# Kernel optimization log

Hardware: AMD Instinct MI355X
Metric: run time of the kernel (lower is better)

Reference implementation:

```python
import jax, jax.numpy as jnp
import numpy as np

INPUT_DIM = 512
HIDDEN_DIM = 1024
OUTPUT_DIM = 1000
BATCH = 256
SEQ_LEN = 256


def setup_inputs() -> dict:
    key = jax.random.key(0)
    ks = jax.random.split(key, 7)
    std = 1.0 / np.sqrt(HIDDEN_DIM)
    u = lambda k, shape: jax.random.uniform(k, shape, jnp.float32, -std, std)
    return {
        "x": jax.random.normal(ks[0], (BATCH, SEQ_LEN, INPUT_DIM), jnp.float32),
        "w_x2h": u(ks[1], (4 * HIDDEN_DIM, INPUT_DIM)),
        "b_x2h": u(ks[2], (4 * HIDDEN_DIM,)),
        "w_h2h": u(ks[3], (4 * HIDDEN_DIM, HIDDEN_DIM)),
        "b_h2h": u(ks[4], (4 * HIDDEN_DIM,)),
        "w_fc": u(ks[5], (OUTPUT_DIM, HIDDEN_DIM)),
        "b_fc": u(ks[6], (OUTPUT_DIM,)),
    }


def _lstm_last_hidden(x, w_x2h, b_x2h, w_h2h, b_h2h):
    B, T, D = x.shape
    H = w_h2h.shape[1]
    # Precompute input-to-hidden for all timesteps in one big GEMM: [B,T,4H]
    xg = jnp.einsum("btd,gd->btg", x, w_x2h) + b_x2h + b_h2h
    xg = jnp.swapaxes(xg, 0, 1)  # [T,B,4H] for scan

    def step(carry, xg_t):
        h, c = carry
        gates = xg_t + h @ w_h2h.T  # [B,4H]
        i, f, g, o = jnp.split(gates, 4, axis=1)
        i = jax.nn.sigmoid(i)
        f = jax.nn.sigmoid(f)
        g = jnp.tanh(g)
        o = jax.nn.sigmoid(o)
        c = c * f + i * g
        h = o * jnp.tanh(c)
        return (h, c), None

    h0 = jnp.zeros((B, H), x.dtype)
    c0 = jnp.zeros((B, H), x.dtype)
    (h_last, _), _ = jax.lax.scan(step, (h0, c0), xg)
    return h_last


def reference(x, w_x2h, b_x2h, w_h2h, b_h2h, w_fc, b_fc):
    h_last = _lstm_last_hidden(x, w_x2h, b_x2h, w_h2h, b_h2h)  # [B,H]
    return h_last @ w_fc.T + b_fc  # [B,OUTPUT_DIM]
```

## Files before the change

kernel.cpp:

```cpp
#include <hip/hip_runtime.h>

typedef __attribute__((ext_vector_type(8))) short short8;
typedef __attribute__((ext_vector_type(4))) float floatx4;

#define DIN  512
#define HSZ  1024
#define G4   4096
#define KTOT 1536
#define BQ   256
#define TT   256

#define MFMA __builtin_amdgcn_mfma_f32_16x16x32_bf16

__device__ __forceinline__ unsigned short f2bf(float f){
  unsigned int u = __float_as_uint(f);
  u += 0x7fffu + ((u >> 16) & 1u);
  return (unsigned short)(u >> 16);
}
__device__ __forceinline__ unsigned int pack2(float a, float b){
  return (unsigned int)f2bf(a) | ((unsigned int)f2bf(b) << 16);
}

__global__ void prep_wcat(const float* __restrict__ wx, const float* __restrict__ wh,
                          const float* __restrict__ bx, const float* __restrict__ bh,
                          unsigned short* __restrict__ Wcat, float* __restrict__ bias){
  int gid = blockIdx.x * blockDim.x + threadIdx.x;
  int idx = gid * 8;
  int g = idx / KTOT;
  int k = idx - g * KTOT;
  const float* src = (k < DIN) ? (wx + (size_t)g * DIN + k)
                               : (wh + (size_t)g * HSZ + (k - DIN));
  float4 f0 = *(const float4*)(src);
  float4 f1 = *(const float4*)(src + 4);
  uint4 v = make_uint4(pack2(f0.x,f0.y), pack2(f0.z,f0.w), pack2(f1.x,f1.y), pack2(f1.z,f1.w));
  *(uint4*)(Wcat + (size_t)g * KTOT + k) = v;
  if (gid < G4) bias[gid] = bx[gid] + bh[gid];
}

__global__ void prep_wfc(const float* __restrict__ wfc, unsigned short* __restrict__ Wfcb){
  int gid = blockIdx.x * blockDim.x + threadIdx.x;
  int idx = gid * 8;
  int n = idx >> 10;
  int k = idx & 1023;
  uint4 v;
  if (n < 1000){
    const float* src = wfc + (size_t)n * 1024 + k;
    float4 f0 = *(const float4*)(src);
    float4 f1 = *(const float4*)(src + 4);
    v = make_uint4(pack2(f0.x,f0.y), pack2(f0.z,f0.w), pack2(f1.x,f1.y), pack2(f1.z,f1.w));
  } else {
    v = make_uint4(0u, 0u, 0u, 0u);
  }
  *(uint4*)(Wfcb + idx) = v;
}

__global__ void prep_x(const float* __restrict__ x, unsigned short* __restrict__ xbf){
  int gid = blockIdx.x * 256 + threadIdx.x;
  int d8 = gid & 63;
  int b  = (gid >> 6) & 255;
  int t  = gid >> 14;
  const float* src = x + (((size_t)b * TT) + t) * DIN + d8 * 8;
  float4 f0 = *(const float4*)(src);
  float4 f1 = *(const float4*)(src + 4);
  uint4 v = make_uint4(pack2(f0.x,f0.y), pack2(f0.z,f0.w), pack2(f1.x,f1.y), pack2(f1.z,f1.w));
  *(uint4*)(xbf + (((size_t)t * BQ) + b) * DIN + d8 * 8) = v;
}

__global__ void init_misc(unsigned int* __restrict__ h0w, unsigned int* __restrict__ cnt, int ncnt){
  int gid = blockIdx.x * 256 + threadIdx.x;
  if (gid < 131072) h0w[gid] = 0u;
  if (gid < ncnt)   cnt[gid] = 0u;
}

__global__ __launch_bounds__(512, 2)
void lstm_persist(const unsigned short* __restrict__ xbf,
                  const unsigned short* __restrict__ Wcat,
                  const float* __restrict__ bias,
                  unsigned short* __restrict__ hseq,
                  unsigned int* __restrict__ cnt){
  extern __shared__ char smem[];
  char*  Ws  = smem;
  float* Gt2 = (float*)(smem + 98304);
  float* Bls = (float*)(smem + 98304 + 34816);

  const int tid  = threadIdx.x;
  const int bx   = blockIdx.x;
  const int bg   = bx >> 7;
  const int b0   = bg << 7;
  const int hb   = bx & 127;
  const int u0   = hb << 3;
  const int lane = tid & 63;
  const int w    = tid >> 6;
  const int rg   = w & 3;
  const int kg   = w >> 2;

  {
    int c  = tid >> 4;
    int ch = tid & 15;
    int g  = c >> 3, j = c & 7;
    const char* src = (const char*)(Wcat + (size_t)(g * HSZ + u0 + j) * KTOT);
    char* dst = Ws + c * 3072;
    int xr = j << 4;
    #pragma unroll
    for (int q = 0; q < 12; ++q){
      int k2 = ch * 192 + q * 16;
      *(uint4*)(dst + (k2 ^ xr)) = *(const uint4*)(src + k2);
    }
    if (tid < 32) Bls[tid] = bias[(size_t)(tid >> 3) * HSZ + u0 + (tid & 7)];
  }
  __syncthreads();

  const int kq8  = (lane >> 4) * 8;
  const int cA   = lane & 15;
  const int cB   = 16 + (lane & 15);
  const char* bpA = Ws + cA * 3072; const int xorA = (cA & 7) << 4;
  const char* bpB = Ws + cB * 3072; const int xorB = (cB & 7) << 4;

  const size_t rowA0 = (size_t)(b0 + rg * 32 + (lane & 15));

  const int erow = tid >> 2;
  const int eup  = (tid & 3) * 2;
  float cst0 = 0.f, cst1 = 0.f;

  for (int t = 0; t < TT; ++t){
    const unsigned short* hin  = hseq + (size_t)t * (BQ * HSZ);
    unsigned short*       hout = hseq + (size_t)(t + 1) * (BQ * HSZ);

    floatx4 acc[2][2][2];
    #pragma unroll
    for (int ab = 0; ab < 2; ++ab)
      #pragma unroll
      for (int rf = 0; rf < 2; ++rf)
        #pragma unroll
        for (int cf = 0; cf < 2; ++cf)
          acc[ab][rf][cf] = (floatx4){0.f,0.f,0.f,0.f};

    short8 X0[8], X1[8];
    {
      const unsigned short* xr0 = xbf + ((size_t)t * BQ + rowA0) * DIN + kg * 256 + kq8;
      const unsigned short* xr1 = xr0 + (size_t)16 * DIN;
      #pragma unroll
      for (int p = 0; p < 8; ++p){
        X0[p] = *(const short8*)(xr0 + p * 32);
        X1[p] = *(const short8*)(xr1 + p * 32);
      }
    }
    __builtin_amdgcn_sched_barrier(0);

    if (t > 0){
      if (tid < 64){
        const unsigned int* cp = &cnt[(((size_t)t * 2 + bg) * 8) * 16];
        const int g16 = (lane & 7) * 16;
        while (true){
          unsigned int v = __hip_atomic_load(cp + g16, __ATOMIC_RELAXED, __HIP_MEMORY_SCOPE_AGENT);
          if (__ballot(v >= 16u) == ~0ull) break;
          __builtin_amdgcn_s_sleep(1);
        }
      }
      __syncthreads();
      asm volatile("" ::: "memory");
    }

    {
      const int bbase = kg * 512 + kq8 * 2;
      short8 bA[2], bB[2];
      bA[0] = *(const short8*)(bpA + ((bbase     ) ^ xorA));
      bB[0] = *(const short8*)(bpB + ((bbase     ) ^ xorB));
      bA[1] = *(const short8*)(bpA + ((bbase + 64) ^ xorA));
      bB[1] = *(const short8*)(bpB + ((bbase + 64) ^ xorB));
      #pragma unroll
      for (int j = 0; j < 8; ++j){
        const int sl = j & 1;
        short8 b0 = bA[sl], b1 = bB[sl];
        if (j < 6){
          int bb = bbase + (j + 2) * 64;
          bA[sl] = *(const short8*)(bpA + (bb ^ xorA));
          bB[sl] = *(const short8*)(bpB + (bb ^ xorB));
        }
        acc[sl][0][0] = MFMA(X0[j], b0, acc[sl][0][0], 0, 0, 0);
        acc[sl][0][1] = MFMA(X0[j], b1, acc[sl][0][1], 0, 0, 0);
        acc[sl][1][0] = MFMA(X1[j], b0, acc[sl][1][0], 0, 0, 0);
        acc[sl][1][1] = MFMA(X1[j], b1, acc[sl][1][1], 0, 0, 0);
      }
    }

    {
      const unsigned short* hr0 = hin + rowA0 * HSZ + kg * 512 + kq8;
      const unsigned short* hr1 = hr0 + (size_t)16 * HSZ;
      short8 A0[16], A1[16];
      #pragma unroll
      for (int p = 0; p < 16; ++p){
        A0[p] = *(const short8*)(hr0 + p * 32);
        A1[p] = *(const short8*)(hr1 + p * 32);
      }
      __builtin_amdgcn_sched_barrier(0);
      const int bbase = 1024 + kg * 1024 + kq8 * 2;
      short8 bA[2], bB[2];
      bA[0] = *(const short8*)(bpA + ((bbase     ) ^ xorA));
      bB[0] = *(const short8*)(bpB + ((bbase     ) ^ xorB));
      bA[1] = *(const short8*)(bpA + ((bbase + 64) ^ xorA));
      bB[1] = *(const short8*)(bpB + ((bbase + 64) ^ xorB));
      #pragma unroll
      for (int j = 0; j < 16; ++j){
        const int sl = j & 1;
        short8 b0 = bA[sl], b1 = bB[sl];
        if (j < 14){
          int bb = bbase + (j + 2) * 64;
          bA[sl] = *(const short8*)(bpA + (bb ^ xorA));
          bB[sl] = *(const short8*)(bpB + (bb ^ xorB));
        }
        acc[sl][0][0] = MFMA(A0[j], b0, acc[sl][0][0], 0, 0, 0);
        acc[sl][0][1] = MFMA(A0[j], b1, acc[sl][0][1], 0, 0, 0);
        acc[sl][1][0] = MFMA(A1[j], b0, acc[sl][1][0], 0, 0, 0);
        acc[sl][1][1] = MFMA(A1[j], b1, acc[sl][1][1], 0, 0, 0);
      }
    }

    {
      float* gdst = Gt2 + kg * (128 * 34);
      int r0 = rg * 32 + (lane >> 4) * 4;
      #pragma unroll
      for (int rf = 0; rf < 2; ++rf){
        floatx4 g0 = acc[0][rf][0] + acc[1][rf][0];
        floatx4 g1 = acc[0][rf][1] + acc[1][rf][1];
        #pragma unroll
        for (int r = 0; r < 4; ++r){
          gdst[(r0 + rf * 16 + r) * 34 + cA] = g0[r];
          gdst[(r0 + rf * 16 + r) * 34 + cB] = g1[r];
        }
      }
    }
    __syncthreads();

    {
      const float* g0p = Gt2 + erow * 34;
      const float* g1p = g0p + 128 * 34;
      float gi0 = g0p[     eup] + g1p[     eup] + Bls[     eup];
      float gf0 = g0p[ 8 + eup] + g1p[ 8 + eup] + Bls[ 8 + eup];
      float gg0 = g0p[16 + eup] + g1p[16 + eup] + Bls[16 + eup];
      float go0 = g0p[24 + eup] + g1p[24 + eup] + Bls[24 + eup];
      float gi1 = g0p[     eup + 1] + g1p[     eup + 1] + Bls[     eup + 1];
      float gf1 = g0p[ 8 + eup + 1] + g1p[ 8 + eup + 1] + Bls[ 8 + eup + 1];
      float gg1 = g0p[16 + eup + 1] + g1p[16 + eup + 1] + Bls[16 + eup + 1];
      float go1 = g0p[24 + eup + 1] + g1p[24 + eup + 1] + Bls[24 + eup + 1];

      float iv0 = 1.f / (1.f + __expf(-gi0));
      float fv0 = 1.f / (1.f + __expf(-gf0));
      float e20 = __expf(-2.f * fmaxf(fminf(gg0, 30.f), -30.f));
      float gv0 = (1.f - e20) / (1.f + e20);
      float ov0 = 1.f / (1.f + __expf(-go0));
      float cn0 = cst0 * fv0 + iv0 * gv0;
      cst0 = cn0;
      float ec0 = __expf(-2.f * fmaxf(fminf(cn0, 30.f), -30.f));
      float hv0 = ov0 * (1.f - ec0) / (1.f + ec0);

      float iv1 = 1.f / (1.f + __expf(-gi1));
      float fv1 = 1.f / (1.f + __expf(-gf1));
      float e21 = __expf(-2.f * fmaxf(fminf(gg1, 30.f), -30.f));
      float gv1 = (1.f - e21) / (1.f + e21);
      float ov1 = 1.f / (1.f + __expf(-go1));
      float cn1 = cst1 * fv1 + iv1 * gv1;
      cst1 = cn1;
      float ec1 = __expf(-2.f * fmaxf(fminf(cn1, 30.f), -30.f));
      float hv1 = ov1 * (1.f - ec1) / (1.f + ec1);

      __hip_atomic_store((unsigned int*)(hout + (size_t)(b0 + erow) * HSZ + u0 + eup),
                         pack2(hv0, hv1), __ATOMIC_RELAXED, __HIP_MEMORY_SCOPE_AGENT);
    }
    __syncthreads();

    if (tid == 0){
      __hip_atomic_fetch_add(&cnt[(((size_t)(t + 1) * 2 + bg) * 8 + (hb >> 4)) * 16], 1u,
                             __ATOMIC_RELAXED, __HIP_MEMORY_SCOPE_AGENT);
    }
  }
}

__global__ __launch_bounds__(256, 1)
void fc_kernel(const unsigned short* __restrict__ h, const unsigned short* __restrict__ wfc,
               const float* __restrict__ bfc, float* __restrict__ out){
  int bx = blockIdx.x, tid = threadIdx.x;
  int wave = tid >> 6, lane = tid & 63;
  int row0 = (bx >> 4) * 64 + wave * 16;
  int col0 = (bx & 15) * 64;
  int lr = lane & 15, lk = (lane >> 4) * 8;
  floatx4 acc[4] = {{0.f,0.f,0.f,0.f},{0.f,0.f,0.f,0.f},{0.f,0.f,0.f,0.f},{0.f,0.f,0.f,0.f}};
  #pragma unroll 4
  for (int ks = 0; ks < 32; ++ks){
    int k = ks * 32 + lk;
    short8 a = *(const short8*)(h + (size_t)(row0 + lr) * 1024 + k);
    #pragma unroll
    for (int fj = 0; fj < 4; ++fj){
      short8 b = *(const short8*)(wfc + (size_t)(col0 + fj * 16 + lr) * 1024 + k);
      acc[fj] = MFMA(a, b, acc[fj], 0, 0, 0);
    }
  }
  #pragma unroll
  for (int fj = 0; fj < 4; ++fj){
    int col = col0 + fj * 16 + lr;
    if (col < 1000){
      #pragma unroll
      for (int r = 0; r < 4; ++r){
        int row = row0 + (lane >> 4) * 4 + r;
        out[(size_t)row * 1000 + col] = acc[fj][r] + bfc[col];
      }
    }
  }
}

extern "C" void kernel_launch(void* const* d_in, const int* in_sizes, int n_in,
                              void* d_out, int out_size, void* d_ws, size_t ws_size,
                              hipStream_t stream){
  const float* x    = (const float*)d_in[0];
  const float* wx2h = (const float*)d_in[1];
  const float* bx2h = (const float*)d_in[2];
  const float* wh2h = (const float*)d_in[3];
  const float* bh2h = (const float*)d_in[4];
  const float* wfc  = (const float*)d_in[5];
  const float* bfc  = (const float*)d_in[6];
  float* out = (float*)d_out;
  char* ws = (char*)d_ws;

  unsigned short* Wcat = (unsigned short*)(ws + 0);
  unsigned short* Wfcb = (unsigned short*)(ws + 12582912);
  float*          bias = (float*)         (ws + 14680064);
  unsigned short* xbf  = (unsigned short*)(ws + 14696448);
  unsigned short* hseq = (unsigned short*)(ws + 81805312);
  unsigned int*   cntb = (unsigned int*)  (ws + 216547328);

  (void)hipFuncSetAttribute((const void*)lstm_persist,
                            hipFuncAttributeMaxDynamicSharedMemorySize, 133376);

  hipLaunchKernelGGL(prep_wcat, dim3(3072), dim3(256), 0, stream, wx2h, wh2h, bx2h, bh2h, Wcat, bias);
  hipLaunchKernelGGL(prep_wfc,  dim3(512),  dim3(256), 0, stream, wfc, Wfcb);
  hipLaunchKernelGGL(prep_x,    dim3(16384),dim3(256), 0, stream, x, xbf);
  hipLaunchKernelGGL(init_misc, dim3(512),  dim3(256), 0, stream,
                     (unsigned int*)hseq, cntb, (int)(263168 / 4));

  hipLaunchKernelGGL(lstm_persist, dim3(256), dim3(512), 133376, stream,
                     xbf, Wcat, bias, hseq, cntb);

  hipLaunchKernelGGL(fc_kernel, dim3(64), dim3(256), 0, stream,
                     hseq + (size_t)256 * BQ * HSZ, Wfcb, bfc, out);
}
```

Baseline: 3.109 ms.

## Overlap next-step input projection with barrier wait and retile persistent LSTM

Each block now owns 64 batch rows by 16 hidden units instead of 128 rows by 8 units, and only W_h2h is kept in LDS. The input projection W_x·x for step t+1 is computed right after h_t is published, using a new k-blocked bf16 copy of W_x read from global memory, so it can overlap the wait for other blocks. Per-block atomic counters are replaced by one flag per block, and each group of 64 blocks waits on its own flags. The split-K reduction goes through LDS with an extra barrier. Costs are more global traffic for W_x every step, more LDS, and extra live registers.

```diff
diff --git a/kernel.cpp b/kernel.cpp
--- a/kernel.cpp
+++ b/kernel.cpp
@@ -37,6 +37,17 @@
   if (gid < G4) bias[gid] = bx[gid] + bh[gid];
 }
 
+__global__ void prep_wxp(const float* __restrict__ wx, unsigned short* __restrict__ WxP){
+  int gid = blockIdx.x * 256 + threadIdx.x;
+  int col = gid >> 6;
+  int kb  = gid & 63;
+  const float* src = wx + (size_t)col * DIN + kb * 8;
+  float4 f0 = *(const float4*)(src);
+  float4 f1 = *(const float4*)(src + 4);
+  uint4 v = make_uint4(pack2(f0.x,f0.y), pack2(f0.z,f0.w), pack2(f1.x,f1.y), pack2(f1.z,f1.w));
+  *(uint4*)(WxP + ((size_t)kb * G4 + col) * 8) = v;
+}
+
 __global__ void prep_wfc(const float* __restrict__ wfc, unsigned short* __restrict__ Wfcb){
   int gid = blockIdx.x * blockDim.x + threadIdx.x;
   int idx = gid * 8;
@@ -66,94 +77,106 @@
   *(uint4*)(xbf + (((size_t)t * BQ) + b) * DIN + d8 * 8) = v;
 }
 
-__global__ void init_misc(unsigned int* __restrict__ h0w, unsigned int* __restrict__ cnt, int ncnt){
+__global__ void init_misc(unsigned int* __restrict__ h0w, unsigned int* __restrict__ flags, int nflags){
   int gid = blockIdx.x * 256 + threadIdx.x;
   if (gid < 131072) h0w[gid] = 0u;
-  if (gid < ncnt)   cnt[gid] = 0u;
+  if (gid < nflags) flags[gid] = 0u;
 }
 
 __global__ __launch_bounds__(512, 2)
 void lstm_persist(const unsigned short* __restrict__ xbf,
                   const unsigned short* __restrict__ Wcat,
+                  const unsigned short* __restrict__ WxP,
                   const float* __restrict__ bias,
                   unsigned short* __restrict__ hseq,
-                  unsigned int* __restrict__ cnt){
+                  unsigned int* __restrict__ flags){
   extern __shared__ char smem[];
   char*  Ws  = smem;
-  float* Gt2 = (float*)(smem + 98304);
-  float* Bls = (float*)(smem + 98304 + 34816);
+  float* Gt  = (float*)(smem + 131072);
+  float* Bls = (float*)(smem + 148480);
 
   const int tid  = threadIdx.x;
   const int bx   = blockIdx.x;
-  const int bg   = bx >> 7;
-  const int b0   = bg << 7;
-  const int hb   = bx & 127;
-  const int u0   = hb << 3;
+  const int bg   = bx >> 6;
+  const int hb6  = bx & 63;
+  const int b0   = bg << 6;
+  const int u0   = hb6 << 4;
   const int lane = tid & 63;
   const int w    = tid >> 6;
-  const int rg   = w & 3;
-  const int kg   = w >> 2;
+  const int kg   = w & 1;
+  const int cg   = (w >> 1) & 1;
+  const int rg   = (w >> 2) & 1;
 
   {
-    int c  = tid >> 4;
-    int ch = tid & 15;
-    int g  = c >> 3, j = c & 7;
-    const char* src = (const char*)(Wcat + (size_t)(g * HSZ + u0 + j) * KTOT);
-    char* dst = Ws + c * 3072;
-    int xr = j << 4;
-    #pragma unroll
-    for (int q = 0; q < 12; ++q){
-      int k2 = ch * 192 + q * 16;
-      *(uint4*)(dst + (k2 ^ xr)) = *(const uint4*)(src + k2);
-    }
-    if (tid < 32) Bls[tid] = bias[(size_t)(tid >> 3) * HSZ + u0 + (tid & 7)];
+    int c  = tid >> 3;
+    int ch = tid & 7;
+    int g = c >> 4, uu = c & 15;
+    const char* src = (const char*)(Wcat + (size_t)(g * HSZ + u0 + uu) * KTOT + DIN);
+    char* dst = Ws + c * 2048;
+    int xr = (c & 7) << 4;
+    #pragma unroll
+    for (int q = 0; q < 16; ++q){
+      int off = ch * 256 + q * 16;
+      *(uint4*)(dst + (off ^ xr)) = *(const uint4*)(src + off);
+    }
+    if (tid < 64) Bls[tid] = bias[(size_t)(tid >> 4) * HSZ + u0 + (tid & 15)];
   }
   __syncthreads();
 
-  const int kq8  = (lane >> 4) * 8;
-  const int cA   = lane & 15;
-  const int cB   = 16 + (lane & 15);
-  const char* bpA = Ws + cA * 3072; const int xorA = (cA & 7) << 4;
-  const char* bpB = Ws + cB * 3072; const int xorB = (cB & 7) << 4;
-
-  const size_t rowA0 = (size_t)(b0 + rg * 32 + (lane & 15));
-
-  const int erow = tid >> 2;
-  const int eup  = (tid & 3) * 2;
+  const int kq8 = (lane >> 4) * 8;
+  const int c0  = cg * 32 + (lane & 15);
+  const int c1  = c0 + 16;
+  const char* bp0 = Ws + c0 * 2048; const int xr0 = (c0 & 7) << 4;
+  const char* bp1 = Ws + c1 * 2048; const int xr1 = (c1 & 7) << 4;
+  const int gcol0 = (c0 >> 4) * HSZ + u0 + (lane & 15);
+  const int gcol1 = (c1 >> 4) * HSZ + u0 + (lane & 15);
+  const int arow  = b0 + rg * 32 + (lane & 15);
+
+  const int er = tid >> 3;
+  const int up = (tid & 7) * 2;
   float cst0 = 0.f, cst1 = 0.f;
+
+  floatx4 xacc[2][2];
+
+  auto compute_x = [&](int t){
+    const unsigned short* xr0p = xbf + ((size_t)t * BQ + arow) * DIN + kg * 256 + kq8;
+    const unsigned short* xr1p = xr0p + 16 * DIN;
+    short8 XA0[8], XA1[8], XB0[8], XB1[8];
+    #pragma unroll
+    for (int j = 0; j < 8; ++j){
+      XA0[j] = *(const short8*)(xr0p + j * 32);
+      XA1[j] = *(const short8*)(xr1p + j * 32);
+      int kb = kg * 32 + j * 4 + (lane >> 4);
+      XB0[j] = *(const short8*)(WxP + ((size_t)kb * G4 + gcol0) * 8);
+      XB1[j] = *(const short8*)(WxP + ((size_t)kb * G4 + gcol1) * 8);
+    }
+    __builtin_amdgcn_sched_barrier(0);
+    #pragma unroll
+    for (int rf = 0; rf < 2; ++rf)
+      #pragma unroll
+      for (int cf = 0; cf < 2; ++cf)
+        xacc[rf][cf] = (floatx4){0.f,0.f,0.f,0.f};
+    #pragma unroll
+    for (int j = 0; j < 8; ++j){
+      xacc[0][0] = MFMA(XA0[j], XB0[j], xacc[0][0], 0, 0, 0);
+      xacc[0][1] = MFMA(XA0[j], XB1[j], xacc[0][1], 0, 0, 0);
+      xacc[1][0] = MFMA(XA1[j], XB0[j], xacc[1][0], 0, 0, 0);
+      xacc[1][1] = MFMA(XA1[j], XB1[j], xacc[1][1], 0, 0, 0);
+    }
+  };
+
+  compute_x(0);
 
   for (int t = 0; t < TT; ++t){
     const unsigned short* hin  = hseq + (size_t)t * (BQ * HSZ);
     unsigned short*       hout = hseq + (size_t)(t + 1) * (BQ * HSZ);
 
-    floatx4 acc[2][2][2];
-    #pragma unroll
-    for (int ab = 0; ab < 2; ++ab)
-      #pragma unroll
-      for (int rf = 0; rf < 2; ++rf)
-        #pragma unroll
-        for (int cf = 0; cf < 2; ++cf)
-          acc[ab][rf][cf] = (floatx4){0.f,0.f,0.f,0.f};
-
-    short8 X0[8], X1[8];
-    {
-      const unsigned short* xr0 = xbf + ((size_t)t * BQ + rowA0) * DIN + kg * 256 + kq8;
-      const unsigned short* xr1 = xr0 + (size_t)16 * DIN;
-      #pragma unroll
-      for (int p = 0; p < 8; ++p){
-        X0[p] = *(const short8*)(xr0 + p * 32);
-        X1[p] = *(const short8*)(xr1 + p * 32);
-      }
-    }
-    __builtin_amdgcn_sched_barrier(0);
-
     if (t > 0){
       if (tid < 64){
-        const unsigned int* cp = &cnt[(((size_t)t * 2 + bg) * 8) * 16];
-        const int g16 = (lane & 7) * 16;
+        const unsigned int* fp = flags + (((size_t)t * 4 + bg) << 6);
         while (true){
-          unsigned int v = __hip_atomic_load(cp + g16, __ATOMIC_RELAXED, __HIP_MEMORY_SCOPE_AGENT);
-          if (__ballot(v >= 16u) == ~0ull) break;
+          unsigned int v = __hip_atomic_load(fp + lane, __ATOMIC_RELAXED, __HIP_MEMORY_SCOPE_AGENT);
+          if (__ballot(v != 0u) == ~0ull) break;
           __builtin_amdgcn_s_sleep(1);
         }
       }
@@ -161,88 +184,83 @@
       asm volatile("" ::: "memory");
     }
 
+    floatx4 hacc[2][2];
+    #pragma unroll
+    for (int rf = 0; rf < 2; ++rf)
+      #pragma unroll
+      for (int cf = 0; cf < 2; ++cf)
+        hacc[rf][cf] = (floatx4){0.f,0.f,0.f,0.f};
     {
-      const int bbase = kg * 512 + kq8 * 2;
-      short8 bA[2], bB[2];
-      bA[0] = *(const short8*)(bpA + ((bbase     ) ^ xorA));
-      bB[0] = *(const short8*)(bpB + ((bbase     ) ^ xorB));
-      bA[1] = *(const short8*)(bpA + ((bbase + 64) ^ xorA));
-      bB[1] = *(const short8*)(bpB + ((bbase + 64) ^ xorB));
-      #pragma unroll
-      for (int j = 0; j < 8; ++j){
-        const int sl = j & 1;
-        short8 b0 = bA[sl], b1 = bB[sl];
-        if (j < 6){
-          int bb = bbase + (j + 2) * 64;
-          bA[sl] = *(const short8*)(bpA + (bb ^ xorA));
-          bB[sl] = *(const short8*)(bpB + (bb ^ xorB));
-        }
-        acc[sl][0][0] = MFMA(X0[j], b0, acc[sl][0][0], 0, 0, 0);
-        acc[sl][0][1] = MFMA(X0[j], b1, acc[sl][0][1], 0, 0, 0);
-        acc[sl][1][0] = MFMA(X1[j], b0, acc[sl][1][0], 0, 0, 0);
-        acc[sl][1][1] = MFMA(X1[j], b1, acc[sl][1][1], 0, 0, 0);
-      }
-    }
-
-    {
-      const unsigned short* hr0 = hin + rowA0 * HSZ + kg * 512 + kq8;
-      const unsigned short* hr1 = hr0 + (size_t)16 * HSZ;
-      short8 A0[16], A1[16];
+      const unsigned short* hr0 = hin + (size_t)arow * HSZ + kg * 512 + kq8;
+      const unsigned short* hr1 = hr0 + 16 * HSZ;
+      short8 HA0[16], HA1[16];
       #pragma unroll
       for (int p = 0; p < 16; ++p){
-        A0[p] = *(const short8*)(hr0 + p * 32);
-        A1[p] = *(const short8*)(hr1 + p * 32);
+        HA0[p] = *(const short8*)(hr0 + p * 32);
+        HA1[p] = *(const short8*)(hr1 + p * 32);
       }
       __builtin_amdgcn_sched_barrier(0);
-      const int bbase = 1024 + kg * 1024 + kq8 * 2;
-      short8 bA[2], bB[2];
-      bA[0] = *(const short8*)(bpA + ((bbase     ) ^ xorA));
-      bB[0] = *(const short8*)(bpB + ((bbase     ) ^ xorB));
-      bA[1] = *(const short8*)(bpA + ((bbase + 64) ^ xorA));
-      bB[1] = *(const short8*)(bpB + ((bbase + 64) ^ xorB));
+      const int kb2 = kg * 1024 + kq8 * 2;
+      short8 B0[2], B1[2];
+      B0[0] = *(const short8*)(bp0 + ((kb2     ) ^ xr0));
+      B1[0] = *(const short8*)(bp1 + ((kb2     ) ^ xr1));
+      B0[1] = *(const short8*)(bp0 + ((kb2 + 64) ^ xr0));
+      B1[1] = *(const short8*)(bp1 + ((kb2 + 64) ^ xr1));
       #pragma unroll
       for (int j = 0; j < 16; ++j){
         const int sl = j & 1;
-        short8 b0 = bA[sl], b1 = bB[sl];
+        short8 b0v = B0[sl], b1v = B1[sl];
         if (j < 14){
-          int bb = bbase + (j + 2) * 64;
-          bA[sl] = *(const short8*)(bpA + (bb ^ xorA));
-          bB[sl] = *(const short8*)(bpB + (bb ^ xorB));
+          int bb = kb2 + (j + 2) * 64;
+          B0[sl] = *(const short8*)(bp0 + (bb ^ xr0));
+          B1[sl] = *(const short8*)(bp1 + (bb ^ xr1));
         }
-        acc[sl][0][0] = MFMA(A0[j], b0, acc[sl][0][0], 0, 0, 0);
-        acc[sl][0][1] = MFMA(A0[j], b1, acc[sl][0][1], 0, 0, 0);
-        acc[sl][1][0] = MFMA(A1[j], b0, acc[sl][1][0], 0, 0, 0);
-        acc[sl][1][1] = MFMA(A1[j], b1, acc[sl][1][1], 0, 0, 0);
-      }
-    }
-
-    {
-      float* gdst = Gt2 + kg * (128 * 34);
-      int r0 = rg * 32 + (lane >> 4) * 4;
+        hacc[0][0] = MFMA(HA0[j], b0v, hacc[0][0], 0, 0, 0);
+        hacc[0][1] = MFMA(HA0[j], b1v, hacc[0][1], 0, 0, 0);
+        hacc[1][0] = MFMA(HA1[j], b0v, hacc[1][0], 0, 0, 0);
+        hacc[1][1] = MFMA(HA1[j], b1v, hacc[1][1], 0, 0, 0);
+      }
+    }
+
+    if (kg == 0){
+      int grow = rg * 32 + (lane >> 4) * 4;
       #pragma unroll
       for (int rf = 0; rf < 2; ++rf){
-        floatx4 g0 = acc[0][rf][0] + acc[1][rf][0];
-        floatx4 g1 = acc[0][rf][1] + acc[1][rf][1];
+        floatx4 gv0 = hacc[rf][0] + xacc[rf][0];
+        floatx4 gv1 = hacc[rf][1] + xacc[rf][1];
         #pragma unroll
         for (int r = 0; r < 4; ++r){
-          gdst[(r0 + rf * 16 + r) * 34 + cA] = g0[r];
-          gdst[(r0 + rf * 16 + r) * 34 + cB] = g1[r];
+          Gt[(grow + rf * 16 + r) * 68 + c0] = gv0[r];
+          Gt[(grow + rf * 16 + r) * 68 + c1] = gv1[r];
         }
       }
     }
     __syncthreads();
+    if (kg == 1){
+      int grow = rg * 32 + (lane >> 4) * 4;
+      #pragma unroll
+      for (int rf = 0; rf < 2; ++rf){
+        floatx4 gv0 = hacc[rf][0] + xacc[rf][0];
+        floatx4 gv1 = hacc[rf][1] + xacc[rf][1];
+        #pragma unroll
+        for (int r = 0; r < 4; ++r){
+          Gt[(grow + rf * 16 + r) * 68 + c0] += gv0[r];
+          Gt[(grow + rf * 16 + r) * 68 + c1] += gv1[r];
+        }
+      }
+    }
+    __syncthreads();
 
     {
-      const float* g0p = Gt2 + erow * 34;
-      const float* g1p = g0p + 128 * 34;
-      float gi0 = g0p[     eup] + g1p[     eup] + Bls[     eup];
-      float gf0 = g0p[ 8 + eup] + g1p[ 8 + eup] + Bls[ 8 + eup];
-      float gg0 = g0p[16 + eup] + g1p[16 + eup] + Bls[16 + eup];
-      float go0 = g0p[24 + eup] + g1p[24 + eup] + Bls[24 + eup];
-      float gi1 = g0p[     eup + 1] + g1p[     eup + 1] + Bls[     eup + 1];
-      float gf1 = g0p[ 8 + eup + 1] + g1p[ 8 + eup + 1] + Bls[ 8 + eup + 1];
-      float gg1 = g0p[16 + eup + 1] + g1p[16 + eup + 1] + Bls[16 + eup + 1];
-      float go1 = g0p[24 + eup + 1] + g1p[24 + eup + 1] + Bls[24 + eup + 1];
+      const float* gr = Gt + er * 68;
+      float gi0 = gr[     up] + Bls[     up];
+      float gf0 = gr[16 + up] + Bls[16 + up];
+      float gg0 = gr[32 + up] + Bls[32 + up];
+      float go0 = gr[48 + up] + Bls[48 + up];
+      float gi1 = gr[     up + 1] + Bls[     up + 1];
+      float gf1 = gr[16 + up + 1] + Bls[16 + up + 1];
+      float gg1 = gr[32 + up + 1] + Bls[32 + up + 1];
+      float go1 = gr[48 + up + 1] + Bls[48 + up + 1];
 
       float iv0 = 1.f / (1.f + __expf(-gi0));
       float fv0 = 1.f / (1.f + __expf(-gf0));
@@ -264,15 +282,16 @@
       float ec1 = __expf(-2.f * fmaxf(fminf(cn1, 30.f), -30.f));
       float hv1 = ov1 * (1.f - ec1) / (1.f + ec1);
 
-      __hip_atomic_store((unsigned int*)(hout + (size_t)(b0 + erow) * HSZ + u0 + eup),
+      __hip_atomic_store((unsigned int*)(hout + (size_t)(b0 + er) * HSZ + u0 + up),
                          pack2(hv0, hv1), __ATOMIC_RELAXED, __HIP_MEMORY_SCOPE_AGENT);
     }
     __syncthreads();
 
-    if (tid == 0){
-      __hip_atomic_fetch_add(&cnt[(((size_t)(t + 1) * 2 + bg) * 8 + (hb >> 4)) * 16], 1u,
-                             __ATOMIC_RELAXED, __HIP_MEMORY_SCOPE_AGENT);
-    }
+    if (tid == 0)
+      __hip_atomic_store(&flags[(((size_t)(t + 1) * 4 + bg) << 6) + hb6], 1u,
+                         __ATOMIC_RELAXED, __HIP_MEMORY_SCOPE_AGENT);
+
+    if (t + 1 < TT) compute_x(t + 1);
   }
 }
 
@@ -321,24 +340,26 @@
   float* out = (float*)d_out;
   char* ws = (char*)d_ws;
 
-  unsigned short* Wcat = (unsigned short*)(ws + 0);
-  unsigned short* Wfcb = (unsigned short*)(ws + 12582912);
-  float*          bias = (float*)         (ws + 14680064);
-  unsigned short* xbf  = (unsigned short*)(ws + 14696448);
-  unsigned short* hseq = (unsigned short*)(ws + 81805312);
-  unsigned int*   cntb = (unsigned int*)  (ws + 216547328);
+  unsigned short* Wcat  = (unsigned short*)(ws + 0);
+  unsigned short* Wfcb  = (unsigned short*)(ws + 12582912);
+  float*          bias  = (float*)         (ws + 14680064);
+  unsigned short* WxP   = (unsigned short*)(ws + 14696448);
+  unsigned short* xbf   = (unsigned short*)(ws + 18890752);
+  unsigned short* hseq  = (unsigned short*)(ws + 85999616);
+  unsigned int*   flags = (unsigned int*)  (ws + 220741632);
 
   (void)hipFuncSetAttribute((const void*)lstm_persist,
-                            hipFuncAttributeMaxDynamicSharedMemorySize, 133376);
+                            hipFuncAttributeMaxDynamicSharedMemorySize, 148736);
 
   hipLaunchKernelGGL(prep_wcat, dim3(3072), dim3(256), 0, stream, wx2h, wh2h, bx2h, bh2h, Wcat, bias);
+  hipLaunchKernelGGL(prep_wxp,  dim3(1024), dim3(256), 0, stream, wx2h, WxP);
   hipLaunchKernelGGL(prep_wfc,  dim3(512),  dim3(256), 0, stream, wfc, Wfcb);
   hipLaunchKernelGGL(prep_x,    dim3(16384),dim3(256), 0, stream, x, xbf);
   hipLaunchKernelGGL(init_misc, dim3(512),  dim3(256), 0, stream,
-                     (unsigned int*)hseq, cntb, (int)(263168 / 4));
-
-  hipLaunchKernelGGL(lstm_persist, dim3(256), dim3(512), 133376, stream,
-                     xbf, Wcat, bias, hseq, cntb);
+                     (unsigned int*)hseq, flags, (int)(263168 / 4));
+
+  hipLaunchKernelGGL(lstm_persist, dim3(256), dim3(512), 148736, stream,
+                     xbf, Wcat, WxP, bias, hseq, flags);
 
   hipLaunchKernelGGL(fc_kernel, dim3(64), dim3(256), 0, stream,
                      hseq + (size_t)256 * BQ * HSZ, Wfcb, bfc, out);
```

Result: slower. 3.437 ms (+10.5%).

## Precompute next step's input projection off the critical path; use per-block step flags

Applied to the files above, without the earlier changes.

The x-projection MFMAs for step t+1 now run right after a block publishes its h for step t, so they overlap with waiting on other blocks instead of sitting inside the dependent chain. The grid barrier changes from per-step atomic counters to per-block monotonic step flags written with plain stores. One wave polls all 128 flags and releases the other waves through a shared-memory mailbox rather than __syncthreads. The wave-to-row/k mapping also changes (kg/rg swapped). The risk is extra live accumulator registers, and spinning waves that contend for issue slots.

```diff
diff --git a/kernel.cpp b/kernel.cpp
--- a/kernel.cpp
+++ b/kernel.cpp
@@ -66,10 +66,10 @@
   *(uint4*)(xbf + (((size_t)t * BQ) + b) * DIN + d8 * 8) = v;
 }
 
-__global__ void init_misc(unsigned int* __restrict__ h0w, unsigned int* __restrict__ cnt, int ncnt){
+__global__ void init_misc(unsigned int* __restrict__ h0w, unsigned int* __restrict__ flags, int nflags){
   int gid = blockIdx.x * 256 + threadIdx.x;
   if (gid < 131072) h0w[gid] = 0u;
-  if (gid < ncnt)   cnt[gid] = 0u;
+  if (gid < nflags) flags[gid] = 0u;
 }
 
 __global__ __launch_bounds__(512, 2)
@@ -77,11 +77,12 @@
                   const unsigned short* __restrict__ Wcat,
                   const float* __restrict__ bias,
                   unsigned short* __restrict__ hseq,
-                  unsigned int* __restrict__ cnt){
+                  unsigned int* __restrict__ flags){
   extern __shared__ char smem[];
   char*  Ws  = smem;
   float* Gt2 = (float*)(smem + 98304);
   float* Bls = (float*)(smem + 98304 + 34816);
+  __shared__ int mbx;
 
   const int tid  = threadIdx.x;
   const int bx   = blockIdx.x;
@@ -91,128 +92,137 @@
   const int u0   = hb << 3;
   const int lane = tid & 63;
   const int w    = tid >> 6;
-  const int rg   = w & 3;
-  const int kg   = w >> 2;
+  const int kg   = w & 1;
+  const int rg   = w >> 1;
 
   {
     int c  = tid >> 4;
     int ch = tid & 15;
-    int g  = c >> 3, j = c & 7;
-    const char* src = (const char*)(Wcat + (size_t)(g * HSZ + u0 + j) * KTOT);
+    int grow = (c >> 3) * HSZ + u0 + (c & 7);
+    const char* src = (const char*)(Wcat + (size_t)grow * KTOT);
     char* dst = Ws + c * 3072;
-    int xr = j << 4;
+    int xr = (c & 7) << 4;
     #pragma unroll
     for (int q = 0; q < 12; ++q){
       int k2 = ch * 192 + q * 16;
       *(uint4*)(dst + (k2 ^ xr)) = *(const uint4*)(src + k2);
     }
     if (tid < 32) Bls[tid] = bias[(size_t)(tid >> 3) * HSZ + u0 + (tid & 7)];
+    if (tid == 0) mbx = 0;
   }
   __syncthreads();
 
-  const int kq8  = (lane >> 4) * 8;
-  const int cA   = lane & 15;
-  const int cB   = 16 + (lane & 15);
+  const int kq8 = (lane >> 4) * 8;
+  const int cA  = lane & 15;
+  const int cB  = 16 + (lane & 15);
   const char* bpA = Ws + cA * 3072; const int xorA = (cA & 7) << 4;
   const char* bpB = Ws + cB * 3072; const int xorB = (cB & 7) << 4;
 
   const size_t rowA0 = (size_t)(b0 + rg * 32 + (lane & 15));
 
-  const int erow = tid >> 2;
-  const int eup  = (tid & 3) * 2;
+  const int er = tid >> 2;
+  const int up = (tid & 3) * 2;
   float cst0 = 0.f, cst1 = 0.f;
+
+  floatx4 xacc[2][2];
+
+  auto compute_x = [&](int t){
+    const unsigned short* xr0p = xbf + ((size_t)t * BQ + rowA0) * DIN + kg * 256 + kq8;
+    const unsigned short* xr1p = xr0p + 16 * DIN;
+    short8 X0[8], X1[8];
+    #pragma unroll
+    for (int p = 0; p < 8; ++p){
+      X0[p] = *(const short8*)(xr0p + p * 32);
+      X1[p] = *(const short8*)(xr1p + p * 32);
+    }
+    __builtin_amdgcn_sched_barrier(0);
+    #pragma unroll
+    for (int rf = 0; rf < 2; ++rf)
+      #pragma unroll
+      for (int cf = 0; cf < 2; ++cf)
+        xacc[rf][cf] = (floatx4){0.f,0.f,0.f,0.f};
+    const int bbase = kg * 512 + kq8 * 2;
+    short8 bA[2], bB[2];
+    bA[0] = *(const short8*)(bpA + ((bbase     ) ^ xorA));
+    bB[0] = *(const short8*)(bpB + ((bbase     ) ^ xorB));
+    bA[1] = *(const short8*)(bpA + ((bbase + 64) ^ xorA));
+    bB[1] = *(const short8*)(bpB + ((bbase + 64) ^ xorB));
+    #pragma unroll
+    for (int j = 0; j < 8; ++j){
+      const int sl = j & 1;
+      short8 b0v = bA[sl], b1v = bB[sl];
+      if (j < 6){
+        int bb = bbase + (j + 2) * 64;
+        bA[sl] = *(const short8*)(bpA + (bb ^ xorA));
+        bB[sl] = *(const short8*)(bpB + (bb ^ xorB));
+      }
+      xacc[0][0] = MFMA(X0[j], b0v, xacc[0][0], 0, 0, 0);
+      xacc[0][1] = MFMA(X0[j], b1v, xacc[0][1], 0, 0, 0);
+      xacc[1][0] = MFMA(X1[j], b0v, xacc[1][0], 0, 0, 0);
+      xacc[1][1] = MFMA(X1[j], b1v, xacc[1][1], 0, 0, 0);
+    }
+  };
+
+  compute_x(0);
+
+  const unsigned int* fz = flags + (bg << 7);
 
   for (int t = 0; t < TT; ++t){
     const unsigned short* hin  = hseq + (size_t)t * (BQ * HSZ);
     unsigned short*       hout = hseq + (size_t)(t + 1) * (BQ * HSZ);
 
-    floatx4 acc[2][2][2];
-    #pragma unroll
-    for (int ab = 0; ab < 2; ++ab)
-      #pragma unroll
-      for (int rf = 0; rf < 2; ++rf)
-        #pragma unroll
-        for (int cf = 0; cf < 2; ++cf)
-          acc[ab][rf][cf] = (floatx4){0.f,0.f,0.f,0.f};
-
-    short8 X0[8], X1[8];
-    {
-      const unsigned short* xr0 = xbf + ((size_t)t * BQ + rowA0) * DIN + kg * 256 + kq8;
-      const unsigned short* xr1 = xr0 + (size_t)16 * DIN;
-      #pragma unroll
-      for (int p = 0; p < 8; ++p){
-        X0[p] = *(const short8*)(xr0 + p * 32);
-        X1[p] = *(const short8*)(xr1 + p * 32);
-      }
-    }
-    __builtin_amdgcn_sched_barrier(0);
-
     if (t > 0){
-      if (tid < 64){
-        const unsigned int* cp = &cnt[(((size_t)t * 2 + bg) * 8) * 16];
-        const int g16 = (lane & 7) * 16;
+      if (w == 0){
         while (true){
-          unsigned int v = __hip_atomic_load(cp + g16, __ATOMIC_RELAXED, __HIP_MEMORY_SCOPE_AGENT);
-          if (__ballot(v >= 16u) == ~0ull) break;
+          unsigned int va = __hip_atomic_load(fz + lane,      __ATOMIC_RELAXED, __HIP_MEMORY_SCOPE_AGENT);
+          unsigned int vb = __hip_atomic_load(fz + 64 + lane, __ATOMIC_RELAXED, __HIP_MEMORY_SCOPE_AGENT);
+          if (__ballot(va >= (unsigned)t && vb >= (unsigned)t) == ~0ull) break;
           __builtin_amdgcn_s_sleep(1);
         }
-      }
-      __syncthreads();
+        if (lane == 0)
+          __hip_atomic_store(&mbx, t, __ATOMIC_RELAXED, __HIP_MEMORY_SCOPE_WORKGROUP);
+      } else {
+        while (__hip_atomic_load(&mbx, __ATOMIC_RELAXED, __HIP_MEMORY_SCOPE_WORKGROUP) < t)
+          __builtin_amdgcn_s_sleep(1);
+      }
       asm volatile("" ::: "memory");
     }
 
+    floatx4 hacc[2][2];
+    #pragma unroll
+    for (int rf = 0; rf < 2; ++rf)
+      #pragma unroll
+      for (int cf = 0; cf < 2; ++cf)
+        hacc[rf][cf] = (floatx4){0.f,0.f,0.f,0.f};
     {
-      const int bbase = kg * 512 + kq8 * 2;
+      const unsigned short* hr0 = hin + rowA0 * HSZ + kg * 512 + kq8;
+      const unsigned short* hr1 = hr0 + 16 * HSZ;
+      short8 HA0[16], HA1[16];
+      #pragma unroll
+      for (int p = 0; p < 16; ++p){
+        HA0[p] = *(const short8*)(hr0 + p * 32);
+        HA1[p] = *(const short8*)(hr1 + p * 32);
+      }
+      __builtin_amdgcn_sched_barrier(0);
+      const int kb2 = 1024 + kg * 1024 + kq8 * 2;
       short8 bA[2], bB[2];
-      bA[0] = *(const short8*)(bpA + ((bbase     ) ^ xorA));
-      bB[0] = *(const short8*)(bpB + ((bbase     ) ^ xorB));
-      bA[1] = *(const short8*)(bpA + ((bbase + 64) ^ xorA));
-      bB[1] = *(const short8*)(bpB + ((bbase + 64) ^ xorB));
-      #pragma unroll
-      for (int j = 0; j < 8; ++j){
+      bA[0] = *(const short8*)(bpA + ((kb2     ) ^ xorA));
+      bB[0] = *(const short8*)(bpB + ((kb2     ) ^ xorB));
+      bA[1] = *(const short8*)(bpA + ((kb2 + 64) ^ xorA));
+      bB[1] = *(const short8*)(bpB + ((kb2 + 64) ^ xorB));
+      #pragma unroll
+      for (int j = 0; j < 16; ++j){
         const int sl = j & 1;
-        short8 b0 = bA[sl], b1 = bB[sl];
-        if (j < 6){
-          int bb = bbase + (j + 2) * 64;
+        short8 b0v = bA[sl], b1v = bB[sl];
+        if (j < 14){
+          int bb = kb2 + (j + 2) * 64;
           bA[sl] = *(const short8*)(bpA + (bb ^ xorA));
           bB[sl] = *(const short8*)(bpB + (bb ^ xorB));
         }
-        acc[sl][0][0] = MFMA(X0[j], b0, acc[sl][0][0], 0, 0, 0);
-        acc[sl][0][1] = MFMA(X0[j], b1, acc[sl][0][1], 0, 0, 0);
-        acc[sl][1][0] = MFMA(X1[j], b0, acc[sl][1][0], 0, 0, 0);
-        acc[sl][1][1] = MFMA(X1[j], b1, acc[sl][1][1], 0, 0, 0);
-      }
-    }
-
-    {
-      const unsigned short* hr0 = hin + rowA0 * HSZ + kg * 512 + kq8;
-      const unsigned short* hr1 = hr0 + (size_t)16 * HSZ;
-      short8 A0[16], A1[16];
-      #pragma unroll
-      for (int p = 0; p < 16; ++p){
-        A0[p] = *(const short8*)(hr0 + p * 32);
-        A1[p] = *(const short8*)(hr1 + p * 32);
-      }
-      __builtin_amdgcn_sched_barrier(0);
-      const int bbase = 1024 + kg * 1024 + kq8 * 2;
-      short8 bA[2], bB[2];
-      bA[0] = *(const short8*)(bpA + ((bbase     ) ^ xorA));
-      bB[0] = *(const short8*)(bpB + ((bbase     ) ^ xorB));
-      bA[1] = *(const short8*)(bpA + ((bbase + 64) ^ xorA));
-      bB[1] = *(const short8*)(bpB + ((bbase + 64) ^ xorB));
-      #pragma unroll
-      for (int j = 0; j < 16; ++j){
-        const int sl = j & 1;
-        short8 b0 = bA[sl], b1 = bB[sl];
-        if (j < 14){
-          int bb = bbase + (j + 2) * 64;
-          bA[sl] = *(const short8*)(bpA + (bb ^ xorA));
-          bB[sl] = *(const short8*)(bpB + (bb ^ xorB));
-        }
-        acc[sl][0][0] = MFMA(A0[j], b0, acc[sl][0][0], 0, 0, 0);
-        acc[sl][0][1] = MFMA(A0[j], b1, acc[sl][0][1], 0, 0, 0);
-        acc[sl][1][0] = MFMA(A1[j], b0, acc[sl][1][0], 0, 0, 0);
-        acc[sl][1][1] = MFMA(A1[j], b1, acc[sl][1][1], 0, 0, 0);
+        hacc[0][0] = MFMA(HA0[j], b0v, hacc[0][0], 0, 0, 0);
+        hacc[0][1] = MFMA(HA0[j], b1v, hacc[0][1], 0, 0, 0);
+        hacc[1][0] = MFMA(HA1[j], b0v, hacc[1][0], 0, 0, 0);
+        hacc[1][1] = MFMA(HA1[j], b1v, hacc[1][1], 0, 0, 0);
       }
     }
 
@@ -221,8 +231,8 @@
       int r0 = rg * 32 + (lane >> 4) * 4;
       #pragma unroll
       for (int rf = 0; rf < 2; ++rf){
-        floatx4 g0 = acc[0][rf][0] + acc[1][rf][0];
-        floatx4 g1 = acc[0][rf][1] + acc[1][rf][1];
+        floatx4 g0 = hacc[rf][0] + xacc[rf][0];
+        floatx4 g1 = hacc[rf][1] + xacc[rf][1];
         #pragma unroll
         for (int r = 0; r < 4; ++r){
           gdst[(r0 + rf * 16 + r) * 34 + cA] = g0[r];
@@ -233,16 +243,16 @@
     __syncthreads();
 
     {
-      const float* g0p = Gt2 + erow * 34;
+      const float* g0p = Gt2 + er * 34;
       const float* g1p = g0p + 128 * 34;
-      float gi0 = g0p[     eup] + g1p[     eup] + Bls[     eup];
-      float gf0 = g0p[ 8 + eup] + g1p[ 8 + eup] + Bls[ 8 + eup];
-      float gg0 = g0p[16 + eup] + g1p[16 + eup] + Bls[16 + eup];
-      float go0 = g0p[24 + eup] + g1p[24 + eup] + Bls[24 + eup];
-      float gi1 = g0p[     eup + 1] + g1p[     eup + 1] + Bls[     eup + 1];
-      float gf1 = g0p[ 8 + eup + 1] + g1p[ 8 + eup + 1] + Bls[ 8 + eup + 1];
-      float gg1 = g0p[16 + eup + 1] + g1p[16 + eup + 1] + Bls[16 + eup + 1];
-      float go1 = g0p[24 + eup + 1] + g1p[24 + eup + 1] + Bls[24 + eup + 1];
+      float gi0 = g0p[     up] + g1p[     up] + Bls[     up];
+      float gf0 = g0p[ 8 + up] + g1p[ 8 + up] + Bls[ 8 + up];
+      float gg0 = g0p[16 + up] + g1p[16 + up] + Bls[16 + up];
+      float go0 = g0p[24 + up] + g1p[24 + up] + Bls[24 + up];
+      float gi1 = g0p[     up + 1] + g1p[     up + 1] + Bls[     up + 1];
+      float gf1 = g0p[ 8 + up + 1] + g1p[ 8 + up + 1] + Bls[ 8 + up + 1];
+      float gg1 = g0p[16 + up + 1] + g1p[16 + up + 1] + Bls[16 + up + 1];
+      float go1 = g0p[24 + up + 1] + g1p[24 + up + 1] + Bls[24 + up + 1];
 
       float iv0 = 1.f / (1.f + __expf(-gi0));
       float fv0 = 1.f / (1.f + __expf(-gf0));
@@ -264,15 +274,16 @@
       float ec1 = __expf(-2.f * fmaxf(fminf(cn1, 30.f), -30.f));
       float hv1 = ov1 * (1.f - ec1) / (1.f + ec1);
 
-      __hip_atomic_store((unsigned int*)(hout + (size_t)(b0 + erow) * HSZ + u0 + eup),
+      __hip_atomic_store((unsigned int*)(hout + (size_t)(b0 + er) * HSZ + u0 + up),
                          pack2(hv0, hv1), __ATOMIC_RELAXED, __HIP_MEMORY_SCOPE_AGENT);
     }
     __syncthreads();
 
-    if (tid == 0){
-      __hip_atomic_fetch_add(&cnt[(((size_t)(t + 1) * 2 + bg) * 8 + (hb >> 4)) * 16], 1u,
-                             __ATOMIC_RELAXED, __HIP_MEMORY_SCOPE_AGENT);
-    }
+    if (tid == 0)
+      __hip_atomic_store((unsigned int*)(fz + hb), (unsigned)(t + 1),
+                         __ATOMIC_RELAXED, __HIP_MEMORY_SCOPE_AGENT);
+
+    if (t + 1 < TT) compute_x(t + 1);
   }
 }
 
@@ -321,12 +332,12 @@
   float* out = (float*)d_out;
   char* ws = (char*)d_ws;
 
-  unsigned short* Wcat = (unsigned short*)(ws + 0);
-  unsigned short* Wfcb = (unsigned short*)(ws + 12582912);
-  float*          bias = (float*)         (ws + 14680064);
-  unsigned short* xbf  = (unsigned short*)(ws + 14696448);
-  unsigned short* hseq = (unsigned short*)(ws + 81805312);
-  unsigned int*   cntb = (unsigned int*)  (ws + 216547328);
+  unsigned short* Wcat  = (unsigned short*)(ws + 0);
+  unsigned short* Wfcb  = (unsigned short*)(ws + 12582912);
+  float*          bias  = (float*)         (ws + 14680064);
+  unsigned short* xbf   = (unsigned short*)(ws + 14696448);
+  unsigned short* hseq  = (unsigned short*)(ws + 81805312);
+  unsigned int*   flags = (unsigned int*)  (ws + 216547328);
 
   (void)hipFuncSetAttribute((const void*)lstm_persist,
                             hipFuncAttributeMaxDynamicSharedMemorySize, 133376);
@@ -335,10 +346,10 @@
   hipLaunchKernelGGL(prep_wfc,  dim3(512),  dim3(256), 0, stream, wfc, Wfcb);
   hipLaunchKernelGGL(prep_x,    dim3(16384),dim3(256), 0, stream, x, xbf);
   hipLaunchKernelGGL(init_misc, dim3(512),  dim3(256), 0, stream,
-                     (unsigned int*)hseq, cntb, (int)(263168 / 4));
+                     (unsigned int*)hseq, flags, 256);
 
   hipLaunchKernelGGL(lstm_persist, dim3(256), dim3(512), 133376, stream,
-                     xbf, Wcat, bias, hseq, cntb);
+                     xbf, Wcat, bias, hseq, flags);
 
   hipLaunchKernelGGL(fc_kernel, dim3(64), dim3(256), 0, stream,
                      hseq + (size_t)256 * BQ * HSZ, Wfcb, bfc, out);
```

Result: slower. 3.775 ms (+21.4%).
